# Optimization experiments

Hardware: AMD Instinct MI355X
Metric: run time of the kernel (lower is better)

## Reference

```python
import jax, jax.numpy as jnp
import numpy as np

B, ATT, CTX = 32, 256, 512
HID = 512
EMB = 256
VOCAB = 5000
T = 161  # seq length; decoder runs T-1 steps


def setup_inputs() -> dict:
    key = jax.random.key(0)
    ks = jax.random.split(key, 32)
    s = 0.02
    p = {}
    p['cnn_feats'] = jax.random.normal(ks[0], (B, ATT, CTX), dtype=jnp.float32)
    p['seq'] = jax.random.randint(ks[1], (B, T), 0, VOCAB, dtype=jnp.int32)
    p['embed'] = jax.random.normal(ks[2], (VOCAB, EMB), dtype=jnp.float32) * s
    # context_embed: Linear(CTX, HID) + ReLU
    p['Wce'] = jax.random.normal(ks[3], (CTX, HID), dtype=jnp.float32) * s
    p['bce'] = jnp.zeros((HID,), jnp.float32)
    # LSTMCell(EMB+CTX, HID): gate order i,f,g,o
    p['Wih'] = jax.random.normal(ks[4], (EMB + CTX, 4 * HID), dtype=jnp.float32) * s
    p['bih'] = jnp.zeros((4 * HID,), jnp.float32)
    p['Whh'] = jax.random.normal(ks[5], (HID, 4 * HID), dtype=jnp.float32) * s
    p['bhh'] = jnp.zeros((4 * HID,), jnp.float32)
    # i2h / h2h
    p['Wi2h'] = jax.random.normal(ks[6], (EMB + CTX, HID), dtype=jnp.float32) * s
    p['bi2h'] = jnp.zeros((HID,), jnp.float32)
    p['Wh2h'] = jax.random.normal(ks[7], (HID, HID), dtype=jnp.float32) * s
    p['bh2h'] = jnp.zeros((HID,), jnp.float32)
    # fr_linear: Linear(HID, CTX) + ReLU ; fr_embed: Linear(CTX, HID)
    p['Wfr'] = jax.random.normal(ks[8], (HID, CTX), dtype=jnp.float32) * s
    p['bfr'] = jnp.zeros((CTX,), jnp.float32)
    p['Wfre'] = jax.random.normal(ks[9], (CTX, HID), dtype=jnp.float32) * s
    p['bfre'] = jnp.zeros((HID,), jnp.float32)
    # ho_linear: Linear(HID, HID) + Tanh ; ho_embed: Linear(HID, HID)
    p['Who'] = jax.random.normal(ks[10], (HID, HID), dtype=jnp.float32) * s
    p['bho'] = jnp.zeros((HID,), jnp.float32)
    p['Whoe'] = jax.random.normal(ks[11], (HID, HID), dtype=jnp.float32) * s
    p['bhoe'] = jnp.zeros((HID,), jnp.float32)
    # alpha_net: Linear(HID, 1)
    p['Wa'] = jax.random.normal(ks[12], (HID, 1), dtype=jnp.float32) * s
    p['ba'] = jnp.zeros((1,), jnp.float32)
    # att2h: Linear(HID, HID)
    p['Watt'] = jax.random.normal(ks[13], (HID, HID), dtype=jnp.float32) * s
    p['batt'] = jnp.zeros((HID,), jnp.float32)
    # logit: Linear(HID, VOCAB)
    p['Wlog'] = jax.random.normal(ks[14], (HID, VOCAB), dtype=jnp.float32) * s
    p['blog'] = jnp.zeros((VOCAB,), jnp.float32)
    return p


def _forward(cnn_feats, seq, embed, Wce, bce, Wih, bih, Whh, bhh, Wi2h, bi2h,
             Wh2h, bh2h, Wfr, bfr, Wfre, bfre, Who, bho, Whoe, bhoe,
             Wa, ba, Watt, batt, Wlog, blog):
    bsz = cnn_feats.shape[0]
    hid = Whh.shape[0]
    ctx = Wce.shape[0]
    # context_embed (dropout disabled: eval mode)
    ctx_embed = jax.nn.relu(jnp.einsum('bac,ch->bah', cnn_feats, Wce) + bce)  # [B, ATT, HID]

    xts = embed[seq[:, :-1]]  # [B, T-1, EMB]
    xts = jnp.swapaxes(xts, 0, 1)  # [T-1, B, EMB]

    def step(carry, xt):
        h, c, prev_out = carry
        inp = jnp.concatenate([xt, prev_out], axis=-1)  # [B, EMB+CTX]
        gates = inp @ Wih + bih + h @ Whh + bhh
        i, f, g, o = jnp.split(gates, 4, axis=-1)
        c_n = jax.nn.sigmoid(f) * c + jax.nn.sigmoid(i) * jnp.tanh(g)
        h_n = jax.nn.sigmoid(o) * jnp.tanh(c_n)
        # sentinel gate
        n5 = inp @ Wi2h + bi2h + h @ Wh2h + bh2h
        fr = jax.nn.sigmoid(n5) * jnp.tanh(c_n)
        fr = jax.nn.relu(fr @ Wfr + bfr)            # [B, CTX]
        fre = fr @ Wfre + bfre                      # [B, HID]
        hol = jnp.tanh(h_n @ Who + bho)             # [B, HID]
        hoe = hol @ Whoe + bhoe                     # [B, HID]
        # attention over [sentinel ; context]  -> att_size + 1 slots
        img_all = jnp.concatenate([fr[:, None, :], cnn_feats], axis=1)       # [B, ATT+1, HID]
        img_all_emb = jnp.concatenate([fre[:, None, :], ctx_embed], axis=1)  # [B, ATT+1, HID]
        hA = jnp.tanh(img_all_emb + hoe[:, None, :])
        scores = jnp.einsum('bah,ho->ba', hA, Wa) + ba[0]  # [B, ATT+1]
        PI = jax.nn.softmax(scores, axis=-1)
        vis = jnp.einsum('ba,bah->bh', PI, img_all)
        out_h = jnp.tanh((vis + hol) @ Watt + batt)
        logp = jax.nn.log_softmax(out_h @ Wlog + blog, axis=-1)
        return (h_n, c_n, out_h), logp

    init = (jnp.zeros((bsz, hid), cnn_feats.dtype),
            jnp.zeros((bsz, hid), cnn_feats.dtype),
            jnp.zeros((bsz, ctx), cnn_feats.dtype))
    _, outs = jax.lax.scan(step, init, xts)  # [T-1, B, VOCAB]
    return jnp.swapaxes(outs, 0, 1)  # [B, T-1, VOCAB]


def reference(cnn_feats, seq, embed, Wce, bce, Wih, bih, Whh, bhh, Wi2h, bi2h,
              Wh2h, bh2h, Wfr, bfr, Wfre, bfre, Who, bho, Whoe, bhoe,
              Wa, ba, Watt, batt, Wlog, blog):
    return _forward(cnn_feats, seq, embed, Wce, bce, Wih, bih, Whh, bhh,
                    Wi2h, bi2h, Wh2h, bh2h, Wfr, bfr, Wfre, bfre, Who, bho,
                    Whoe, bhoe, Wa, ba, Watt, batt, Wlog, blog)
```

## Files before the change

kernel.cpp:

```cpp
#include <hip/hip_runtime.h>


typedef unsigned short u16;
typedef unsigned long long u64;
typedef __attribute__((ext_vector_type(8))) short s8;
typedef __attribute__((ext_vector_type(4))) float f4;

#define TT 160
#define NBLK 240

static constexpr size_t oZB   = 0;
static constexpr size_t oC    = 81920;
static constexpr size_t oFLAG = 212992;
static constexpr size_t oSLOT = 213504;
static constexpr size_t oREL  = 215488;
static constexpr size_t ZERO_END = 217088;
static constexpr size_t oWT1  = 217088;
static constexpr size_t oWT2  = 6770688;
static constexpr size_t oWT3  = 11898880;
static constexpr size_t oBG   = 12947456;
static constexpr size_t oXE   = 12957696;
static constexpr size_t oCE   = 15579136;
static constexpr size_t oCW   = 23967744;
static constexpr size_t oGP0  = 32356352;
static constexpr size_t oGP1  = 32684032;
static constexpr size_t oLP0  = 33011712;
static constexpr size_t oLP1  = 33652736;
static constexpr size_t oAB1  = 34293760;
static constexpr size_t oAB2  = 34359296;
static constexpr size_t oV4   = 34424832;
static constexpr size_t oW45T = 34686976;
static constexpr size_t oW6T  = 36784128;

__device__ __forceinline__ float b2f(u16 u){ return __uint_as_float(((unsigned)u) << 16); }
__device__ __forceinline__ u16 f2b(float f){
  unsigned x = __float_as_uint(f);
  return (u16)((x + 0x7fffu + ((x >> 16) & 1u)) >> 16);
}
__device__ __forceinline__ float sigm(float x){ return 1.0f/(1.0f + __expf(-x)); }
__device__ __forceinline__ float tanhp(float x){ return 1.0f - 2.0f/(__expf(2.0f*x) + 1.0f); }
__device__ __forceinline__ u16 rdb(const void* p, size_t i, int f){
  return f ? f2b(((const float*)p)[i]) : ((const u16*)p)[i];
}
__device__ __forceinline__ float rdf(const void* p, size_t i, int f){
  return f ? ((const float*)p)[i] : b2f(((const u16*)p)[i]);
}

__device__ __forceinline__ float ldf(const float* p){
  return __hip_atomic_load((float*)p, __ATOMIC_RELAXED, __HIP_MEMORY_SCOPE_AGENT);
}
__device__ __forceinline__ void stf(float* p, float v){
  __hip_atomic_store(p, v, __ATOMIC_RELAXED, __HIP_MEMORY_SCOPE_AGENT);
}
__device__ __forceinline__ u64 ld64(const void* p){
  return __hip_atomic_load((u64*)p, __ATOMIC_RELAXED, __HIP_MEMORY_SCOPE_AGENT);
}
__device__ __forceinline__ void st64(void* p, u64 v){
  __hip_atomic_store((u64*)p, v, __ATOMIC_RELAXED, __HIP_MEMORY_SCOPE_AGENT);
}
__device__ __forceinline__ s8 ld128(const void* p){
  union { u64 q[2]; s8 v; } u;
  u.q[0] = ld64(p);
  u.q[1] = ld64((const char*)p + 8);
  return u.v;
}

__device__ __forceinline__ void gbar(unsigned* slots, unsigned* rel, unsigned& gen){
  ++gen;
  __syncthreads();
  asm volatile("s_waitcnt vmcnt(0)" ::: "memory");
  if (blockIdx.x == 0){
    const int tid = threadIdx.x;
    if (tid > 0 && tid < NBLK){
      while (__hip_atomic_load(slots + tid*2, __ATOMIC_RELAXED, __HIP_MEMORY_SCOPE_AGENT) < gen)
        __builtin_amdgcn_s_sleep(1);
    }
    __syncthreads();
    if (tid == 0)
      __hip_atomic_store(rel, gen, __ATOMIC_RELAXED, __HIP_MEMORY_SCOPE_AGENT);
  } else {
    if (threadIdx.x == 0){
      __hip_atomic_store(slots + blockIdx.x*2, gen, __ATOMIC_RELAXED, __HIP_MEMORY_SCOPE_AGENT);
      while (__hip_atomic_load(rel, __ATOMIC_RELAXED, __HIP_MEMORY_SCOPE_AGENT) < gen)
        __builtin_amdgcn_s_sleep(1);
    }
    __syncthreads();
  }
}

__global__ void probek(const u16* __restrict__ a, int* flag){
  __shared__ int s[256];
  int t = threadIdx.x;
  float v = fabsf(b2f(a[t]));
  s[t] = (v < 64.0f) ? 0 : 1;
  __syncthreads();
  for (int o = 128; o; o >>= 1){ if (t < o) s[t] += s[t+o]; __syncthreads(); }
  if (t == 0) *flag = (s[0] > 0) ? 1 : 0;
}

__global__ void tposek(const void* __restrict__ src, u16* __restrict__ dst,
                       int R, int C, int stride, const int* __restrict__ flag){
  __shared__ u16 tl[32][33];
  const int f = *flag;
  int nt = blockIdx.x*32, kt = blockIdx.y*32;
  int tx = threadIdx.x & 31, ty = threadIdx.x >> 5;
  #pragma unroll
  for (int i = 0; i < 4; i++){
    int k = kt + ty + i*8, n = nt + tx;
    tl[ty + i*8][tx] = (k < R && n < C) ? rdb(src, (size_t)k*C + n, f) : (u16)0;
  }
  __syncthreads();
  #pragma unroll
  for (int i = 0; i < 4; i++){
    int n = nt + ty + i*8, k = kt + tx;
    if (n < C && k < R) dst[(size_t)n*stride + k] = tl[tx][ty + i*8];
  }
}

__global__ void biask(const void* bih, const void* bhh, const void* bi2h, const void* bh2h,
                      float* bg, const int* __restrict__ flag){
  const int f = *flag;
  int n = blockIdx.x*256 + threadIdx.x;
  if (n >= 2560) return;
  if (n < 2048) bg[n] = rdf(bih, n, f) + rdf(bhh, n, f);
  else { int j = n - 2048; bg[n] = rdf(bi2h, j, f) + rdf(bh2h, j, f); }
}

__global__ void xembk(const int* __restrict__ seq, const void* __restrict__ embed,
                      u16* __restrict__ xe, u16* __restrict__ zb,
                      const int* __restrict__ flag){
  const int f = *flag;
  int t = blockIdx.x, b = blockIdx.y, e = threadIdx.x;
  int idx = seq[b*161 + t];
  u16 v = rdb(embed, (size_t)idx*256 + e, f);
  xe[((size_t)t*32 + b)*256 + e] = v;
  if (t == 0) zb[(size_t)b*1280 + e] = v;
}

__global__ __launch_bounds__(256) void ctxgemm(const void* __restrict__ A,
                                               const u16* __restrict__ WT3,
                                               const void* __restrict__ bce,
                                               u16* __restrict__ CE, u16* __restrict__ CW,
                                               const int* __restrict__ flag){
  const int f = *flag;
  int wave = threadIdx.x >> 6, lane = threadIdx.x & 63;
  int job = blockIdx.x*4 + wave;
  int mq = job >> 4, nq = job & 15;
  int m0 = mq*64, n0 = nq*64;
  int lr = lane & 15, lq = lane >> 4;
  f4 acc[4][4] = {};
  for (int ks = 0; ks < 16; ks++){
    int k0 = ks*32 + lq*8;
    s8 a[4], b[4];
    #pragma unroll
    for (int mt = 0; mt < 4; mt++){
      size_t base = (size_t)(m0 + mt*16 + lr)*512 + k0;
      if (f){
        const float4* ap = (const float4*)((const float*)A + base);
        float4 q0 = ap[0], q1 = ap[1];
        union { u16 u[8]; s8 v; } pk;
        pk.u[0]=f2b(q0.x); pk.u[1]=f2b(q0.y); pk.u[2]=f2b(q0.z); pk.u[3]=f2b(q0.w);
        pk.u[4]=f2b(q1.x); pk.u[5]=f2b(q1.y); pk.u[6]=f2b(q1.z); pk.u[7]=f2b(q1.w);
        a[mt] = pk.v;
      } else {
        a[mt] = *(const s8*)((const u16*)A + base);
      }
    }
    #pragma unroll
    for (int nt = 0; nt < 4; nt++) b[nt] = *(const s8*)(WT3 + (size_t)(n0 + nt*16 + lr)*512 + k0);
    #pragma unroll
    for (int mt = 0; mt < 4; mt++)
      #pragma unroll
      for (int nt = 0; nt < 4; nt++)
        acc[mt][nt] = __builtin_amdgcn_mfma_f32_16x16x32_bf16(a[mt], b[nt], acc[mt][nt], 0, 0, 0);
  }
  #pragma unroll
  for (int mt = 0; mt < 4; mt++)
    #pragma unroll
    for (int nt = 0; nt < 4; nt++)
      #pragma unroll
      for (int r = 0; r < 4; r++){
        int row = m0 + mt*16 + lq*4 + r;
        int col = n0 + nt*16 + lr;
        float d = acc[mt][nt][r];
        if (col < 512){ d += rdf(bce, col, f); d = d > 0.f ? d : 0.f; CE[(size_t)row*512 + col] = f2b(d); }
        else CW[(size_t)row*512 + (col - 512)] = f2b(d);
      }
}

struct DP {
  const void *bfr, *bfre, *bho, *bhoe, *Wa, *batt, *blog;
  const u16 *WT1, *WT2, *xe, *CE, *CW, *w45, *w6;
  const float *bg;
  const int *flag;
  u16 *zb, *ab1, *ab2; float *cbuf, *v4;
  float *gp0, *gp1, *lp0, *lp1;
  float *vp, *ms;
  unsigned *slots, *rel;
  void *out;
};

__global__ __launch_bounds__(256) void loopk(DP p){
  const int blk = blockIdx.x;
  const int tid = threadIdx.x, lane = tid & 63, wv = tid >> 6;
  const int lr = lane & 15, lq = lane >> 4;
  const int f = *p.flag;
  unsigned gen = 0;

  __shared__ float sHOE[512], sWa[512], sP[64], sRED[256], sV[4][512];
  __shared__ u16 sPK[2048];

  for (int t = 0; t <= TT; ++t){
    {
      const int gwave = blk*4 + wv;
      if (t < TT && gwave < 320){
        const int nt = gwave >> 1, kh = gwave & 1;
        const u16* Bp = p.WT1 + (size_t)(nt*16 + lr)*1280 + kh*640 + lq*8;
        const u16* Ap = p.zb + (size_t)lr*1280 + kh*640 + lq*8;
        f4 a0 = {0,0,0,0}, a1 = {0,0,0,0};
        #pragma unroll 4
        for (int ks = 0; ks < 20; ++ks){
          s8 fa0 = ld128(Ap + ks*32);
          s8 fa1 = ld128(Ap + 16*1280 + ks*32);
          s8 fb  = *(const s8*)(Bp + ks*32);
          a0 = __builtin_amdgcn_mfma_f32_16x16x32_bf16(fa0, fb, a0, 0, 0, 0);
          a1 = __builtin_amdgcn_mfma_f32_16x16x32_bf16(fa1, fb, a1, 0, 0, 0);
        }
        float* gp = kh ? p.gp1 : p.gp0;
        const int col = nt*16 + lr, r0 = lq*4;
        #pragma unroll
        for (int r = 0; r < 4; ++r){
          stf(gp + (size_t)(r0 + r)*2560 + col, a0[r]);
          stf(gp + (size_t)(16 + r0 + r)*2560 + col, a1[r]);
        }
      } else if (t > 0 && gwave >= 320 && gwave < 946){
        const int j = gwave - 320, nt = j >> 1, kh = j & 1;
        const u16* Bp = p.WT2 + (size_t)(nt*16 + lr)*512 + kh*256 + lq*8;
        const u16* Ap = p.zb + 256 + (size_t)lr*1280 + kh*256 + lq*8;
        f4 a0 = {0,0,0,0}, a1 = {0,0,0,0};
        #pragma unroll
        for (int ks = 0; ks < 8; ++ks){
          s8 fa0 = ld128(Ap + ks*32);
          s8 fa1 = ld128(Ap + 16*1280 + ks*32);
          s8 fb  = *(const s8*)(Bp + ks*32);
          a0 = __builtin_amdgcn_mfma_f32_16x16x32_bf16(fa0, fb, a0, 0, 0, 0);
          a1 = __builtin_amdgcn_mfma_f32_16x16x32_bf16(fa1, fb, a1, 0, 0, 0);
        }
        float* lp = kh ? p.lp1 : p.lp0;
        const int col = nt*16 + lr, r0 = lq*4;
        #pragma unroll
        for (int r = 0; r < 4; ++r){
          stf(lp + (size_t)(r0 + r)*5008 + col, a0[r]);
          stf(lp + (size_t)(16 + r0 + r)*5008 + col, a1[r]);
        }
      }
    }
    gbar(p.slots, p.rel, gen);

    if (t > 0 && blk < 32){
      const int b = blk;
      const float* l0 = p.lp0 + (size_t)b*5008;
      const float* l1 = p.lp1 + (size_t)b*5008;
      float x[20];
      float m = -3.0e38f;
      #pragma unroll
      for (int i = 0; i < 20; i++){
        int v = tid + i*256;
        x[i] = (v < 5000) ? (ldf(l0 + v) + ldf(l1 + v) + rdf(p.blog, v, f)) : -3.0e38f;
        m = fmaxf(m, x[i]);
      }
      sRED[tid] = m; __syncthreads();
      for (int off = 128; off; off >>= 1){ if (tid < off) sRED[tid] = fmaxf(sRED[tid], sRED[tid+off]); __syncthreads(); }
      float M = sRED[0]; __syncthreads();
      float s = 0.f;
      #pragma unroll
      for (int i = 0; i < 20; i++){ int v = tid + i*256; if (v < 5000) s += __expf(x[i] - M); }
      sRED[tid] = s; __syncthreads();
      for (int off = 128; off; off >>= 1){ if (tid < off) sRED[tid] += sRED[tid+off]; __syncthreads(); }
      float lse = M + __logf(sRED[0]);
      const size_t ob = ((size_t)b*160 + (t-1))*5000;
      if (f){
        float* op = (float*)p.out;
        #pragma unroll
        for (int i = 0; i < 20; i++){ int v = tid + i*256; if (v < 5000) op[ob + v] = x[i] - lse; }
      } else {
        u16* op = (u16*)p.out;
        #pragma unroll
        for (int i = 0; i < 20; i++){ int v = tid + i*256; if (v < 5000) op[ob + v] = f2b(x[i] - lse); }
      }
    } else if (t < TT && blk >= 32 && blk < 64){
      const int b = blk - 32;
      const float* cold = p.cbuf + (size_t)(t & 1)*16384 + (size_t)b*512;
      float*       cnew = p.cbuf + (size_t)((t + 1) & 1)*16384 + (size_t)b*512;
      const float* g0 = p.gp0 + (size_t)b*2560;
      const float* g1 = p.gp1 + (size_t)b*2560;
      #pragma unroll
      for (int i = 0; i < 2; i++){
        const int j = tid + i*256;
        float gi = ldf(g0 + j)        + ldf(g1 + j)        + p.bg[j];
        float gf = ldf(g0 + 512 + j)  + ldf(g1 + 512 + j)  + p.bg[512+j];
        float gg = ldf(g0 + 1024 + j) + ldf(g1 + 1024 + j) + p.bg[1024+j];
        float go = ldf(g0 + 1536 + j) + ldf(g1 + 1536 + j) + p.bg[1536+j];
        float g5 = ldf(g0 + 2048 + j) + ldf(g1 + 2048 + j) + p.bg[2048+j];
        float cn = sigm(gf)*cold[j] + sigm(gi)*tanhp(gg);
        float tc = tanhp(cn);
        float hn = sigm(go)*tc;
        sPK[j]       = f2b(sigm(g5)*tc);
        sPK[512 + j] = f2b(hn);
        cnew[j] = cn;
      }
      __syncthreads();
      st64(p.ab1 + (size_t)b*1024 + tid*4, *(const u64*)(sPK + tid*4));
      if (tid < 128)
        st64(p.zb + (size_t)b*1280 + 768 + tid*4, *(const u64*)(sPK + 512 + tid*4));
      if (t < TT - 1 && tid < 64){
        u64 q = *(const u64*)(p.xe + ((size_t)(t + 1)*32 + b)*256 + tid*4);
        st64(p.zb + (size_t)b*1280 + tid*4, q);
      }
    }
    if (t == TT) break;
    gbar(p.slots, p.rel, gen);

    if (blk < 16){
      const int job = blk*4 + wv;
      const int n0 = job*16;
      const u16* Bp = p.w45 + (size_t)(n0 + lr)*1024 + lq*8;
      const u16* Ap = p.ab1 + (size_t)lr*1024 + lq*8;
      f4 a0 = {0,0,0,0}, a1 = {0,0,0,0};
      #pragma unroll 8
      for (int ks = 0; ks < 32; ++ks){
        s8 fa0 = ld128(Ap + ks*32);
        s8 fa1 = ld128(Ap + 16*1024 + ks*32);
        s8 fb  = *(const s8*)(Bp + ks*32);
        a0 = __builtin_amdgcn_mfma_f32_16x16x32_bf16(fa0, fb, a0, 0, 0, 0);
        a1 = __builtin_amdgcn_mfma_f32_16x16x32_bf16(fa1, fb, a1, 0, 0, 0);
      }
      const int col = n0 + lr, r0 = lq*4;
      const int lcol = wv*16 + lr;
      #pragma unroll
      for (int r = 0; r < 4; ++r){
        float v0 = a0[r], v1 = a1[r];
        if (col < 512){ float bb = rdf(p.bfr, col, f); v0 = fmaxf(v0 + bb, 0.f); v1 = fmaxf(v1 + bb, 0.f); }
        else          { float bb = rdf(p.bho, col - 512, f); v0 = tanhp(v0 + bb); v1 = tanhp(v1 + bb); }
        sPK[(r0 + r)*64 + lcol]      = f2b(v0);
        sPK[(16 + r0 + r)*64 + lcol] = f2b(v1);
      }
      __syncthreads();
      const int row = tid >> 3, c0 = (tid & 7)*8;
      const u16* s = sPK + row*64 + c0;
      u16* dstp = p.ab2 + (size_t)row*1024 + blk*64 + c0;
      st64(dstp,     *(const u64*)s);
      st64(dstp + 4, *(const u64*)(s + 4));
    }
    gbar(p.slots, p.rel, gen);

    if (blk < 32){
      const int job = blk*4 + wv;
      const int n0 = job*16;
      const u16* Bp = p.w6 + (size_t)(n0 + lr)*1024 + lq*8;
      const u16* Ap = p.ab2 + (size_t)lr*1024 + lq*8;
      f4 a0 = {0,0,0,0}, a1 = {0,0,0,0};
      #pragma unroll 8
      for (int ks = 0; ks < 32; ++ks){
        s8 fa0 = ld128(Ap + ks*32);
        s8 fa1 = ld128(Ap + 16*1024 + ks*32);
        s8 fb  = *(const s8*)(Bp + ks*32);
        a0 = __builtin_amdgcn_mfma_f32_16x16x32_bf16(fa0, fb, a0, 0, 0, 0);
        a1 = __builtin_amdgcn_mfma_f32_16x16x32_bf16(fa1, fb, a1, 0, 0, 0);
      }
      const int col = n0 + lr, r0 = lq*4;
      float add = 0.f;
      if (col < 512)        add = rdf(p.bfre, col, f);
      else if (col < 1024)  add = rdf(p.bhoe, col - 512, f);
      #pragma unroll
      for (int r = 0; r < 4; ++r){
        stf(p.v4 + (size_t)(r0 + r)*2048 + col,      a0[r] + add);
        stf(p.v4 + (size_t)(16 + r0 + r)*2048 + col, a1[r] + add);
      }
    }
    gbar(p.slots, p.rel, gen);

    if (blk < 224){
      const int b = blk / 7, jj = blk % 7;
      const int a0 = jj*37;
      const int a1 = (a0 + 37 < 257) ? (a0 + 37) : 257;
      const float* v4 = p.v4 + (size_t)b*2048;
      for (int i = tid; i < 512; i += 256){
        sHOE[i] = ldf(v4 + 512 + i); sWa[i] = rdf(p.Wa, i, f);
      }
      __syncthreads();
      const int h0 = lane*8;
      #pragma unroll 2
      for (int a = a0 + wv; a < a1; a += 4){
        float pp = 0.f;
        if (a == 0){
          #pragma unroll
          for (int j8 = 0; j8 < 8; ++j8){ int h = h0 + j8; pp += tanhp(ldf(v4 + h) + sHOE[h]) * sWa[h]; }
        } else {
          s8 c8 = *(const s8*)(p.CE + ((size_t)b*256 + (a - 1))*512 + h0);
          #pragma unroll
          for (int j8 = 0; j8 < 8; ++j8){ int h = h0 + j8; pp += tanhp(b2f((u16)c8[j8]) + sHOE[h]) * sWa[h]; }
        }
        #pragma unroll
        for (int o = 32; o; o >>= 1) pp += __shfl_xor(pp, o, 64);
        if (lane == 0) sP[a - a0] = __expf(pp);
      }
      __syncthreads();
      {
        float acc[8] = {0,0,0,0,0,0,0,0};
        #pragma unroll 2
        for (int a = a0 + wv; a < a1; a += 4){
          float wgt = sP[a - a0];
          if (a == 0){
            #pragma unroll
            for (int j8 = 0; j8 < 8; ++j8) acc[j8] += wgt * ldf(v4 + 1024 + h0 + j8);
          } else {
            s8 c8 = *(const s8*)(p.CW + ((size_t)b*256 + (a - 1))*512 + h0);
            #pragma unroll
            for (int j8 = 0; j8 < 8; ++j8) acc[j8] += wgt * b2f((u16)c8[j8]);
          }
        }
        #pragma unroll
        for (int j8 = 0; j8 < 8; ++j8) sV[wv][h0 + j8] = acc[j8];
      }
      __syncthreads();
      #pragma unroll
      for (int i = 0; i < 2; ++i){
        int col = tid + i*256;
        stf(p.vp + ((size_t)b*7 + jj)*512 + col,
            sV[0][col] + sV[1][col] + sV[2][col] + sV[3][col]);
      }
      if (tid == 0){
        float s = 0.f;
        for (int k = 0; k < a1 - a0; ++k) s += sP[k];
        stf(p.ms + b*7 + jj, s);
      }
    }
    gbar(p.slots, p.rel, gen);

    if (blk < 32){
      const int b = blk;
      const float* v4 = p.v4 + (size_t)b*2048;
      float S = 0.f;
      #pragma unroll
      for (int k = 0; k < 7; ++k) S += ldf(p.ms + b*7 + k);
      float rS = 1.0f / S;
      #pragma unroll
      for (int i = 0; i < 2; ++i){
        int col = tid + i*256;
        float V = 0.f;
        #pragma unroll
        for (int k = 0; k < 7; ++k) V += ldf(p.vp + ((size_t)b*7 + k)*512 + col);
        float s = V*rS + ldf(v4 + 1536 + col) + rdf(p.batt, col, f);
        sPK[col] = f2b(tanhp(s));
      }
      __syncthreads();
      if (tid < 128)
        st64(p.zb + (size_t)b*1280 + 256 + tid*4, *(const u64*)(sPK + tid*4));
    }
    gbar(p.slots, p.rel, gen);
  }
}

extern "C" void kernel_launch(void* const* d_in, const int* in_sizes, int n_in,
                              void* d_out, int out_size, void* d_ws, size_t ws_size,
                              hipStream_t stream){
  char* w = (char*)d_ws;
  u16*   ZB  = (u16*)(w + oZB);
  float* CB  = (float*)(w + oC);
  int*   FLAG= (int*)(w + oFLAG);
  u16*   WT1 = (u16*)(w + oWT1);
  u16*   WT2 = (u16*)(w + oWT2);
  u16*   WT3 = (u16*)(w + oWT3);
  float* BG  = (float*)(w + oBG);
  u16*   XE  = (u16*)(w + oXE);
  u16*   CE  = (u16*)(w + oCE);
  u16*   CW  = (u16*)(w + oCW);
  u16*   W45T= (u16*)(w + oW45T);
  u16*   W6T = (u16*)(w + oW6T);

  (void)hipMemsetAsync(w, 0, ZERO_END, stream);
  (void)hipMemsetAsync(w + oWT2, 0, (size_t)5008*512*2, stream);
  (void)hipMemsetAsync(w + oW45T, 0, (size_t)(2097152 + 4194304), stream);

  const int* seq  = (const int*)d_in[1];

  probek<<<1, 256, 0, stream>>>((const u16*)d_in[0], FLAG);

  auto T = [&](const void* src, u16* dst, int R, int C, int stride){
    tposek<<<dim3((C + 31)/32, (R + 31)/32), 256, 0, stream>>>(src, dst, R, C, stride, FLAG);
  };
  T(d_in[5],  WT1,                              768, 2048, 1280);
  T(d_in[7],  WT1 + 768,                        512, 2048, 1280);
  T(d_in[9],  WT1 + (size_t)2048*1280,          768,  512, 1280);
  T(d_in[11], WT1 + (size_t)2048*1280 + 768,    512,  512, 1280);
  T(d_in[25], WT2,                              512, 5000,  512);
  T(d_in[3],  WT3,                              512,  512,  512);
  T(d_in[23], WT3 + (size_t)512*512,            512,  512,  512);
  T(d_in[13], W45T,                             512,  512, 1024);
  T(d_in[17], W45T + (size_t)512*1024 + 512,    512,  512, 1024);
  T(d_in[15], W6T,                              512,  512, 1024);
  T(d_in[19], W6T + (size_t)512*1024 + 512,     512,  512, 1024);
  T(d_in[23], W6T + (size_t)1024*1024,          512,  512, 1024);
  T(d_in[23], W6T + (size_t)1536*1024 + 512,    512,  512, 1024);

  biask<<<10, 256, 0, stream>>>(d_in[6], d_in[8], d_in[10], d_in[12], BG, FLAG);
  xembk<<<dim3(160, 32), 256, 0, stream>>>(seq, d_in[2], XE, ZB, FLAG);
  ctxgemm<<<512, 256, 0, stream>>>(d_in[0], WT3, d_in[4], CE, CW, FLAG);

  DP p;
  p.bfr  = d_in[14]; p.bfre = d_in[16];
  p.bho  = d_in[18]; p.bhoe = d_in[20];
  p.Wa   = d_in[21]; p.batt = d_in[24];
  p.blog = d_in[26];
  p.WT1 = WT1; p.WT2 = WT2; p.xe = XE; p.CE = CE; p.CW = CW;
  p.w45 = W45T; p.w6 = W6T;
  p.bg = BG; p.flag = FLAG; p.zb = ZB; p.cbuf = CB;
  p.ab1 = (u16*)(w + oAB1); p.ab2 = (u16*)(w + oAB2);
  p.v4  = (float*)(w + oV4);
  p.gp0 = (float*)(w + oGP0); p.gp1 = (float*)(w + oGP1);
  p.lp0 = (float*)(w + oLP0); p.lp1 = (float*)(w + oLP1);
  p.vp  = (float*)(w + oGP0);
  p.ms  = (float*)(w + oGP0 + 458752);
  p.slots = (unsigned*)(w + oSLOT);
  p.rel   = (unsigned*)(w + oREL);
  p.out = d_out;

  loopk<<<NBLK, 256, 0, stream>>>(p);
}
```

Before: 13.17 ms.

## Replace global barriers with per-block stage flags and dataflow waits

Removes the centralized grid barrier and its release flag. Each block now stamps a per-stage counter, and consumers wait only on the specific producer blocks they depend on. Work is remapped onto fixed block ranges (LSTM gates on blocks 0-79, logits on 80-236, cell update and MLPs on 32-63), so the softmax, gate GEMM and logit GEMM stages can overlap across timesteps. The change also trims the grid to 237 blocks and fully unrolls the attention loops with guards. The risk is subtle ordering or WAR hazards, since workspace buffers such as gp0 (reused for vp/ms) are now shared without a full barrier between stages.

```diff
diff --git a/kernel.cpp b/kernel.cpp
--- a/kernel.cpp
+++ b/kernel.cpp
@@ -7,13 +7,12 @@
 typedef __attribute__((ext_vector_type(4))) float f4;
 
 #define TT 160
-#define NBLK 240
+#define NBLK 237
 
 static constexpr size_t oZB   = 0;
 static constexpr size_t oC    = 81920;
 static constexpr size_t oFLAG = 212992;
 static constexpr size_t oSLOT = 213504;
-static constexpr size_t oREL  = 215488;
 static constexpr size_t ZERO_END = 217088;
 static constexpr size_t oWT1  = 217088;
 static constexpr size_t oWT2  = 6770688;
@@ -65,27 +64,17 @@
   return u.v;
 }
 
-__device__ __forceinline__ void gbar(unsigned* slots, unsigned* rel, unsigned& gen){
-  ++gen;
+__device__ __forceinline__ void stampw(int* slots, int val){
+  asm volatile("s_waitcnt vmcnt(0)" ::: "memory");
   __syncthreads();
-  asm volatile("s_waitcnt vmcnt(0)" ::: "memory");
-  if (blockIdx.x == 0){
-    const int tid = threadIdx.x;
-    if (tid > 0 && tid < NBLK){
-      while (__hip_atomic_load(slots + tid*2, __ATOMIC_RELAXED, __HIP_MEMORY_SCOPE_AGENT) < gen)
-        __builtin_amdgcn_s_sleep(1);
-    }
-    __syncthreads();
-    if (tid == 0)
-      __hip_atomic_store(rel, gen, __ATOMIC_RELAXED, __HIP_MEMORY_SCOPE_AGENT);
-  } else {
-    if (threadIdx.x == 0){
-      __hip_atomic_store(slots + blockIdx.x*2, gen, __ATOMIC_RELAXED, __HIP_MEMORY_SCOPE_AGENT);
-      while (__hip_atomic_load(rel, __ATOMIC_RELAXED, __HIP_MEMORY_SCOPE_AGENT) < gen)
-        __builtin_amdgcn_s_sleep(1);
-    }
-    __syncthreads();
-  }
+  if (threadIdx.x == 0)
+    __hip_atomic_store(slots + (size_t)blockIdx.x*2, val, __ATOMIC_RELAXED, __HIP_MEMORY_SCOPE_AGENT);
+}
+__device__ __forceinline__ void waitset(int* slots, int base, int count, int target){
+  for (int s = threadIdx.x; s < count; s += 256)
+    while (__hip_atomic_load(slots + (size_t)(base + s)*2, __ATOMIC_RELAXED, __HIP_MEMORY_SCOPE_AGENT) < target)
+      __builtin_amdgcn_s_sleep(1);
+  __syncthreads();
 }
 
 __global__ void probek(const u16* __restrict__ a, int* flag){
@@ -196,7 +185,7 @@
   u16 *zb, *ab1, *ab2; float *cbuf, *v4;
   float *gp0, *gp1, *lp0, *lp1;
   float *vp, *ms;
-  unsigned *slots, *rel;
+  int *slots;
   void *out;
 };
 
@@ -205,20 +194,22 @@
   const int tid = threadIdx.x, lane = tid & 63, wv = tid >> 6;
   const int lr = lane & 15, lq = lane >> 4;
   const int f = *p.flag;
-  unsigned gen = 0;
+  int* slots = p.slots;
 
   __shared__ float sHOE[512], sWa[512], sP[64], sRED[256], sV[4][512];
   __shared__ u16 sPK[2048];
 
   for (int t = 0; t <= TT; ++t){
-    {
-      const int gwave = blk*4 + wv;
-      if (t < TT && gwave < 320){
+    const int s6 = t*6;
+    if (blk < 80){
+      waitset(slots, 32, 32, s6);
+      if (t < TT){
+        const int gwave = blk*4 + wv;
         const int nt = gwave >> 1, kh = gwave & 1;
         const u16* Bp = p.WT1 + (size_t)(nt*16 + lr)*1280 + kh*640 + lq*8;
         const u16* Ap = p.zb + (size_t)lr*1280 + kh*640 + lq*8;
         f4 a0 = {0,0,0,0}, a1 = {0,0,0,0};
-        #pragma unroll 4
+        #pragma unroll 5
         for (int ks = 0; ks < 20; ++ks){
           s8 fa0 = ld128(Ap + ks*32);
           s8 fa1 = ld128(Ap + 16*1280 + ks*32);
@@ -233,96 +224,112 @@
           stf(gp + (size_t)(r0 + r)*2560 + col, a0[r]);
           stf(gp + (size_t)(16 + r0 + r)*2560 + col, a1[r]);
         }
-      } else if (t > 0 && gwave >= 320 && gwave < 946){
-        const int j = gwave - 320, nt = j >> 1, kh = j & 1;
-        const u16* Bp = p.WT2 + (size_t)(nt*16 + lr)*512 + kh*256 + lq*8;
-        const u16* Ap = p.zb + 256 + (size_t)lr*1280 + kh*256 + lq*8;
-        f4 a0 = {0,0,0,0}, a1 = {0,0,0,0};
-        #pragma unroll
-        for (int ks = 0; ks < 8; ++ks){
-          s8 fa0 = ld128(Ap + ks*32);
-          s8 fa1 = ld128(Ap + 16*1280 + ks*32);
-          s8 fb  = *(const s8*)(Bp + ks*32);
-          a0 = __builtin_amdgcn_mfma_f32_16x16x32_bf16(fa0, fb, a0, 0, 0, 0);
-          a1 = __builtin_amdgcn_mfma_f32_16x16x32_bf16(fa1, fb, a1, 0, 0, 0);
-        }
-        float* lp = kh ? p.lp1 : p.lp0;
-        const int col = nt*16 + lr, r0 = lq*4;
-        #pragma unroll
-        for (int r = 0; r < 4; ++r){
-          stf(lp + (size_t)(r0 + r)*5008 + col, a0[r]);
-          stf(lp + (size_t)(16 + r0 + r)*5008 + col, a1[r]);
-        }
-      }
-    }
-    gbar(p.slots, p.rel, gen);
-
-    if (t > 0 && blk < 32){
-      const int b = blk;
-      const float* l0 = p.lp0 + (size_t)b*5008;
-      const float* l1 = p.lp1 + (size_t)b*5008;
-      float x[20];
-      float m = -3.0e38f;
-      #pragma unroll
-      for (int i = 0; i < 20; i++){
-        int v = tid + i*256;
-        x[i] = (v < 5000) ? (ldf(l0 + v) + ldf(l1 + v) + rdf(p.blog, v, f)) : -3.0e38f;
-        m = fmaxf(m, x[i]);
-      }
-      sRED[tid] = m; __syncthreads();
-      for (int off = 128; off; off >>= 1){ if (tid < off) sRED[tid] = fmaxf(sRED[tid], sRED[tid+off]); __syncthreads(); }
-      float M = sRED[0]; __syncthreads();
-      float s = 0.f;
-      #pragma unroll
-      for (int i = 0; i < 20; i++){ int v = tid + i*256; if (v < 5000) s += __expf(x[i] - M); }
-      sRED[tid] = s; __syncthreads();
-      for (int off = 128; off; off >>= 1){ if (tid < off) sRED[tid] += sRED[tid+off]; __syncthreads(); }
-      float lse = M + __logf(sRED[0]);
-      const size_t ob = ((size_t)b*160 + (t-1))*5000;
-      if (f){
-        float* op = (float*)p.out;
-        #pragma unroll
-        for (int i = 0; i < 20; i++){ int v = tid + i*256; if (v < 5000) op[ob + v] = x[i] - lse; }
-      } else {
-        u16* op = (u16*)p.out;
-        #pragma unroll
-        for (int i = 0; i < 20; i++){ int v = tid + i*256; if (v < 5000) op[ob + v] = f2b(x[i] - lse); }
-      }
-    } else if (t < TT && blk >= 32 && blk < 64){
-      const int b = blk - 32;
-      const float* cold = p.cbuf + (size_t)(t & 1)*16384 + (size_t)b*512;
-      float*       cnew = p.cbuf + (size_t)((t + 1) & 1)*16384 + (size_t)b*512;
-      const float* g0 = p.gp0 + (size_t)b*2560;
-      const float* g1 = p.gp1 + (size_t)b*2560;
-      #pragma unroll
-      for (int i = 0; i < 2; i++){
-        const int j = tid + i*256;
-        float gi = ldf(g0 + j)        + ldf(g1 + j)        + p.bg[j];
-        float gf = ldf(g0 + 512 + j)  + ldf(g1 + 512 + j)  + p.bg[512+j];
-        float gg = ldf(g0 + 1024 + j) + ldf(g1 + 1024 + j) + p.bg[1024+j];
-        float go = ldf(g0 + 1536 + j) + ldf(g1 + 1536 + j) + p.bg[1536+j];
-        float g5 = ldf(g0 + 2048 + j) + ldf(g1 + 2048 + j) + p.bg[2048+j];
-        float cn = sigm(gf)*cold[j] + sigm(gi)*tanhp(gg);
-        float tc = tanhp(cn);
-        float hn = sigm(go)*tc;
-        sPK[j]       = f2b(sigm(g5)*tc);
-        sPK[512 + j] = f2b(hn);
-        cnew[j] = cn;
-      }
-      __syncthreads();
-      st64(p.ab1 + (size_t)b*1024 + tid*4, *(const u64*)(sPK + tid*4));
-      if (tid < 128)
-        st64(p.zb + (size_t)b*1280 + 768 + tid*4, *(const u64*)(sPK + 512 + tid*4));
-      if (t < TT - 1 && tid < 64){
-        u64 q = *(const u64*)(p.xe + ((size_t)(t + 1)*32 + b)*256 + tid*4);
-        st64(p.zb + (size_t)b*1280 + tid*4, q);
-      }
+      }
+      stampw(slots, s6 + 1);
+    } else {
+      if (t > 0){
+        waitset(slots, 32, 32, s6);
+        waitset(slots, 0, 32, s6 - 4);
+        const int gwave = blk*4 + wv;
+        if (gwave < 946){
+          const int j = gwave - 320, nt = j >> 1, kh = j & 1;
+          const u16* Bp = p.WT2 + (size_t)(nt*16 + lr)*512 + kh*256 + lq*8;
+          const u16* Ap = p.zb + 256 + (size_t)lr*1280 + kh*256 + lq*8;
+          f4 a0 = {0,0,0,0}, a1 = {0,0,0,0};
+          #pragma unroll
+          for (int ks = 0; ks < 8; ++ks){
+            s8 fa0 = ld128(Ap + ks*32);
+            s8 fa1 = ld128(Ap + 16*1280 + ks*32);
+            s8 fb  = *(const s8*)(Bp + ks*32);
+            a0 = __builtin_amdgcn_mfma_f32_16x16x32_bf16(fa0, fb, a0, 0, 0, 0);
+            a1 = __builtin_amdgcn_mfma_f32_16x16x32_bf16(fa1, fb, a1, 0, 0, 0);
+          }
+          float* lp = kh ? p.lp1 : p.lp0;
+          const int col = nt*16 + lr, r0 = lq*4;
+          #pragma unroll
+          for (int r = 0; r < 4; ++r){
+            stf(lp + (size_t)(r0 + r)*5008 + col, a0[r]);
+            stf(lp + (size_t)(16 + r0 + r)*5008 + col, a1[r]);
+          }
+        }
+      }
+      stampw(slots, s6 + 1);
+    }
+
+    if (blk < 32){
+      if (t > 0){
+        waitset(slots, 80, 157, s6 + 1);
+        const int b = blk;
+        const float* l0 = p.lp0 + (size_t)b*5008;
+        const float* l1 = p.lp1 + (size_t)b*5008;
+        float x[20];
+        float m = -3.0e38f;
+        #pragma unroll
+        for (int i = 0; i < 20; i++){
+          int v = tid + i*256;
+          x[i] = (v < 5000) ? (ldf(l0 + v) + ldf(l1 + v) + rdf(p.blog, v, f)) : -3.0e38f;
+          m = fmaxf(m, x[i]);
+        }
+        sRED[tid] = m; __syncthreads();
+        for (int off = 128; off; off >>= 1){ if (tid < off) sRED[tid] = fmaxf(sRED[tid], sRED[tid+off]); __syncthreads(); }
+        float M = sRED[0]; __syncthreads();
+        float s = 0.f;
+        #pragma unroll
+        for (int i = 0; i < 20; i++){ int v = tid + i*256; if (v < 5000) s += __expf(x[i] - M); }
+        sRED[tid] = s; __syncthreads();
+        for (int off = 128; off; off >>= 1){ if (tid < off) sRED[tid] += sRED[tid+off]; __syncthreads(); }
+        float lse = M + __logf(sRED[0]);
+        const size_t ob = ((size_t)b*160 + (t-1))*5000;
+        if (f){
+          float* op = (float*)p.out;
+          #pragma unroll
+          for (int i = 0; i < 20; i++){ int v = tid + i*256; if (v < 5000) op[ob + v] = x[i] - lse; }
+        } else {
+          u16* op = (u16*)p.out;
+          #pragma unroll
+          for (int i = 0; i < 20; i++){ int v = tid + i*256; if (v < 5000) op[ob + v] = f2b(x[i] - lse); }
+        }
+      }
+      stampw(slots, s6 + 2);
+    } else if (blk < 64){
+      if (t < TT){
+        waitset(slots, 0, 80, s6 + 1);
+        const int b = blk - 32;
+        const float* cold = p.cbuf + (size_t)(t & 1)*16384 + (size_t)b*512;
+        float*       cnew = p.cbuf + (size_t)((t + 1) & 1)*16384 + (size_t)b*512;
+        const float* g0 = p.gp0 + (size_t)b*2560;
+        const float* g1 = p.gp1 + (size_t)b*2560;
+        #pragma unroll
+        for (int i = 0; i < 2; i++){
+          const int j = tid + i*256;
+          float gi = ldf(g0 + j)        + ldf(g1 + j)        + p.bg[j];
+          float gf = ldf(g0 + 512 + j)  + ldf(g1 + 512 + j)  + p.bg[512+j];
+          float gg = ldf(g0 + 1024 + j) + ldf(g1 + 1024 + j) + p.bg[1024+j];
+          float go = ldf(g0 + 1536 + j) + ldf(g1 + 1536 + j) + p.bg[1536+j];
+          float g5 = ldf(g0 + 2048 + j) + ldf(g1 + 2048 + j) + p.bg[2048+j];
+          float cn = sigm(gf)*cold[j] + sigm(gi)*tanhp(gg);
+          float tc = tanhp(cn);
+          float hn = sigm(go)*tc;
+          sPK[j]       = f2b(sigm(g5)*tc);
+          sPK[512 + j] = f2b(hn);
+          cnew[j] = cn;
+        }
+        __syncthreads();
+        st64(p.ab1 + (size_t)b*1024 + tid*4, *(const u64*)(sPK + tid*4));
+        if (tid < 128)
+          st64(p.zb + (size_t)b*1280 + 768 + tid*4, *(const u64*)(sPK + 512 + tid*4));
+        if (t < TT - 1 && tid < 64){
+          u64 q = *(const u64*)(p.xe + ((size_t)(t + 1)*32 + b)*256 + tid*4);
+          st64(p.zb + (size_t)b*1280 + tid*4, q);
+        }
+      }
+      stampw(slots, s6 + 2);
     }
     if (t == TT) break;
-    gbar(p.slots, p.rel, gen);
-
-    if (blk < 16){
-      const int job = blk*4 + wv;
+
+    if (blk >= 32 && blk < 48){
+      waitset(slots, 32, 32, s6 + 2);
+      const int job = (blk - 32)*4 + wv;
       const int n0 = job*16;
       const u16* Bp = p.w45 + (size_t)(n0 + lr)*1024 + lq*8;
       const u16* Ap = p.ab1 + (size_t)lr*1024 + lq*8;
@@ -348,14 +355,15 @@
       __syncthreads();
       const int row = tid >> 3, c0 = (tid & 7)*8;
       const u16* s = sPK + row*64 + c0;
-      u16* dstp = p.ab2 + (size_t)row*1024 + blk*64 + c0;
+      u16* dstp = p.ab2 + (size_t)row*1024 + (blk - 32)*64 + c0;
       st64(dstp,     *(const u64*)s);
       st64(dstp + 4, *(const u64*)(s + 4));
-    }
-    gbar(p.slots, p.rel, gen);
-
-    if (blk < 32){
-      const int job = blk*4 + wv;
+      stampw(slots, s6 + 3);
+    }
+
+    if (blk >= 32 && blk < 64){
+      waitset(slots, 32, 16, s6 + 3);
+      const int job = (blk - 32)*4 + wv;
       const int n0 = job*16;
       const u16* Bp = p.w6 + (size_t)(n0 + lr)*1024 + lq*8;
       const u16* Ap = p.ab2 + (size_t)lr*1024 + lq*8;
@@ -377,10 +385,11 @@
         stf(p.v4 + (size_t)(r0 + r)*2048 + col,      a0[r] + add);
         stf(p.v4 + (size_t)(16 + r0 + r)*2048 + col, a1[r] + add);
       }
-    }
-    gbar(p.slots, p.rel, gen);
+      stampw(slots, s6 + 4);
+    }
 
     if (blk < 224){
+      waitset(slots, 32, 32, s6 + 4);
       const int b = blk / 7, jj = blk % 7;
       const int a0 = jj*37;
       const int a1 = (a0 + 37 < 257) ? (a0 + 37) : 257;
@@ -390,34 +399,40 @@
       }
       __syncthreads();
       const int h0 = lane*8;
-      #pragma unroll 2
-      for (int a = a0 + wv; a < a1; a += 4){
-        float pp = 0.f;
-        if (a == 0){
+      #pragma unroll
+      for (int k = 0; k < 10; ++k){
+        int a = a0 + wv + k*4;
+        if (a < a1){
+          float pp = 0.f;
+          if (a == 0){
+            #pragma unroll
+            for (int j8 = 0; j8 < 8; ++j8){ int h = h0 + j8; pp += tanhp(ldf(v4 + h) + sHOE[h]) * sWa[h]; }
+          } else {
+            s8 c8 = *(const s8*)(p.CE + ((size_t)b*256 + (a - 1))*512 + h0);
+            #pragma unroll
+            for (int j8 = 0; j8 < 8; ++j8){ int h = h0 + j8; pp += tanhp(b2f((u16)c8[j8]) + sHOE[h]) * sWa[h]; }
+          }
           #pragma unroll
-          for (int j8 = 0; j8 < 8; ++j8){ int h = h0 + j8; pp += tanhp(ldf(v4 + h) + sHOE[h]) * sWa[h]; }
-        } else {
-          s8 c8 = *(const s8*)(p.CE + ((size_t)b*256 + (a - 1))*512 + h0);
-          #pragma unroll
-          for (int j8 = 0; j8 < 8; ++j8){ int h = h0 + j8; pp += tanhp(b2f((u16)c8[j8]) + sHOE[h]) * sWa[h]; }
-        }
-        #pragma unroll
-        for (int o = 32; o; o >>= 1) pp += __shfl_xor(pp, o, 64);
-        if (lane == 0) sP[a - a0] = __expf(pp);
+          for (int o = 32; o; o >>= 1) pp += __shfl_xor(pp, o, 64);
+          if (lane == 0) sP[a - a0] = __expf(pp);
+        }
       }
       __syncthreads();
       {
         float acc[8] = {0,0,0,0,0,0,0,0};
-        #pragma unroll 2
-        for (int a = a0 + wv; a < a1; a += 4){
-          float wgt = sP[a - a0];
-          if (a == 0){
-            #pragma unroll
-            for (int j8 = 0; j8 < 8; ++j8) acc[j8] += wgt * ldf(v4 + 1024 + h0 + j8);
-          } else {
-            s8 c8 = *(const s8*)(p.CW + ((size_t)b*256 + (a - 1))*512 + h0);
-            #pragma unroll
-            for (int j8 = 0; j8 < 8; ++j8) acc[j8] += wgt * b2f((u16)c8[j8]);
+        #pragma unroll
+        for (int k = 0; k < 10; ++k){
+          int a = a0 + wv + k*4;
+          if (a < a1){
+            float wgt = sP[a - a0];
+            if (a == 0){
+              #pragma unroll
+              for (int j8 = 0; j8 < 8; ++j8) acc[j8] += wgt * ldf(v4 + 1024 + h0 + j8);
+            } else {
+              s8 c8 = *(const s8*)(p.CW + ((size_t)b*256 + (a - 1))*512 + h0);
+              #pragma unroll
+              for (int j8 = 0; j8 < 8; ++j8) acc[j8] += wgt * b2f((u16)c8[j8]);
+            }
           }
         }
         #pragma unroll
@@ -435,11 +450,13 @@
         for (int k = 0; k < a1 - a0; ++k) s += sP[k];
         stf(p.ms + b*7 + jj, s);
       }
-    }
-    gbar(p.slots, p.rel, gen);
-
-    if (blk < 32){
-      const int b = blk;
+      stampw(slots, s6 + 5);
+    }
+
+    if (blk >= 32 && blk < 64){
+      waitset(slots, 0, 224, s6 + 5);
+      waitset(slots, 224, 13, s6 + 1);
+      const int b = blk - 32;
       const float* v4 = p.v4 + (size_t)b*2048;
       float S = 0.f;
       #pragma unroll
@@ -457,8 +474,8 @@
       __syncthreads();
       if (tid < 128)
         st64(p.zb + (size_t)b*1280 + 256 + tid*4, *(const u64*)(sPK + tid*4));
-    }
-    gbar(p.slots, p.rel, gen);
+      stampw(slots, s6 + 6);
+    }
   }
 }
 
@@ -522,8 +539,7 @@
   p.lp0 = (float*)(w + oLP0); p.lp1 = (float*)(w + oLP1);
   p.vp  = (float*)(w + oGP0);
   p.ms  = (float*)(w + oGP0 + 458752);
-  p.slots = (unsigned*)(w + oSLOT);
-  p.rel   = (unsigned*)(w + oREL);
+  p.slots = (int*)(w + oSLOT);
   p.out = d_out;
 
   loopk<<<NBLK, 256, 0, stream>>>(p);
```

After: 13.74 ms. 1.04x slower.
